# Performance work log

Measured on AMD Instinct MI355X. Metric: run time of the kernel, lower is better.

Reference implementation:

```python
import math
import jax, jax.numpy as jnp
import numpy as np

EPS = 1e-4
FMAX = 18  # max filtersize for scale clamped to 2.5: ceil(3*2^2.5+0.5)=18 -> kernel 37x37
KSZ = 2 * FMAX + 1


def _conv2d(x, w, b):
    # 3x3 conv, padding 1, NCHW / OIHW (cross-correlation, matches torch)
    y = jax.lax.conv_general_dilated(x, w, (1, 1), [(1, 1), (1, 1)],
                                     dimension_numbers=('NCHW', 'OIHW', 'NCHW'))
    return y + b[None, :, None, None]


def _basis_filters(scale):
    # scale: [B] -> [B,3,K,K] (g, dgdx, dgdy), masked to the per-sample support
    std = 2.0 ** scale                              # [B]
    fs = jnp.ceil(3.0 * std + 0.5)                  # per-sample filtersize
    x = jnp.arange(-FMAX, FMAX + 1, dtype=jnp.float32)          # [K]
    m = (jnp.abs(x)[None, :] <= fs[:, None]).astype(jnp.float32)  # [B,K] support mask
    e = jnp.exp(-0.5 * (x[None, :] / std[:, None]) ** 2) * m      # masked 1D gaussian [B,K]
    g = e[:, :, None] * e[:, None, :]                              # [B,K,K]
    g = g / jnp.sum(g, axis=(1, 2), keepdims=True)
    c = (-x[None, :] / (std[:, None] ** 3 * 2.0 * math.pi)) * e    # [B,K]
    dgdx = c[:, :, None] * e[:, None, :]   # varies along first spatial dim (x[0])
    dgdx = dgdx / jnp.sum(jnp.abs(dgdx), axis=(1, 2), keepdims=True)
    dgdy = e[:, :, None] * c[:, None, :]   # varies along second spatial dim (x[1])
    dgdy = dgdy / jnp.sum(jnp.abs(dgdy), axis=(1, 2), keepdims=True)
    return jnp.stack([g, dgdx, dgdy], axis=1)  # [B,3,K,K]


def setup_inputs() -> dict:
    key = jax.random.key(0)
    ks = jax.random.split(key, 7)
    B, H, W = 8, 512, 512
    batch = jax.random.uniform(ks[0], (B, 3, H, W), dtype=jnp.float32)
    gcm = jnp.array([[0.06, 0.63, 0.27], [0.3, 0.04, -0.35], [0.34, -0.6, 0.17]],
                    dtype=jnp.float32)
    w1 = jax.random.normal(ks[1], (16, 3, 3, 3), dtype=jnp.float32) * 0.1
    b1 = jax.random.normal(ks[2], (16,), dtype=jnp.float32) * 0.01
    w2 = jax.random.normal(ks[3], (16, 16, 3, 3), dtype=jnp.float32) * 0.1
    b2 = jax.random.normal(ks[4], (16,), dtype=jnp.float32) * 0.01
    w3 = jax.random.normal(ks[5], (1, 16, 3, 3), dtype=jnp.float32) * 0.1
    b3 = jax.random.normal(ks[6], (1,), dtype=jnp.float32) * 0.01
    return {"batch": batch, "gcm": gcm, "w1": w1, "b1": b1,
            "w2": w2, "b2": b2, "w3": w3, "b3": b3}


def reference(batch, gcm, w1, b1, w2, b2, w3, b3):
    B, _, H, W = batch.shape
    # ---- RGB order prior (non-differentiable, no_grad in torch) ----
    oh = lambda i: jax.nn.one_hot(i, 3, axis=1, dtype=batch.dtype)
    mx = jnp.argmax(batch, axis=1)                 # first max
    mn = jnp.argmin(batch, axis=1)
    bf = batch[:, ::-1]
    mx2 = 2 - jnp.argmax(bf, axis=1)               # last max
    mn2 = 2 - jnp.argmin(bf, axis=1)
    RGB_order = jax.lax.stop_gradient(
        0.5 * (oh(mx) + oh(mx2)) - 0.5 * (oh(mn) + oh(mn2)))  # [B,3,H,W]

    # ---- per-sample adaptive scale from small CNN ----
    h = jax.nn.silu(_conv2d(batch, w1, b1))
    h = jax.nn.silu(_conv2d(h, w2, b2))
    s = _conv2d(h, w3, b3)
    scale = jnp.clip(jnp.mean(s, axis=(1, 2, 3)), -2.5, 2.5)   # [B]

    # ---- Gaussian color model ----
    xg = jnp.einsum('ij,bjhw->bihw', gcm, batch)  # [B,3,H,W] -> (E, El, Ell)

    # ---- per-sample Gaussian basis convolution, batched via grouped conv ----
    basis = _basis_filters(scale)                                  # [B,3,K,K]
    xin = xg.reshape(1, B * 3, H, W)
    wk = jnp.broadcast_to(basis[:, None], (B, 3, 3, KSZ, KSZ)).reshape(B * 9, 1, KSZ, KSZ)
    out = jax.lax.conv_general_dilated(xin, wk, (1, 1), [(FMAX, FMAX), (FMAX, FMAX)],
                                       feature_group_count=B * 3,
                                       dimension_numbers=('NCHW', 'OIHW', 'NCHW'))
    out = out.reshape(B, 3, 3, H, W)   # [B, chan(E/El/Ell), filt(g/dx/dy), H, W]
    E = out[:, 0, 0:1]
    Ex = out[:, 0, 1:2]
    Ey = out[:, 0, 2:3]
    El = out[:, 1, 0:1]
    Ell = out[:, 2, 0:1]

    Hf = jnp.arctan(El / (Ell + EPS))
    S = jnp.log((El ** 2 + Ell ** 2) / (E ** 2 + EPS) + EPS)
    Ww = jnp.arctan((Ex / (E + EPS)) ** 2 + (Ey / (E + EPS)) ** 2)
    return jnp.concatenate([Hf, S, RGB_order, Ww], axis=1)  # [B,6,H,W]
```

## Files before the change

### kernel.cpp

```cpp
#include <hip/hip_runtime.h>
#include <hip/hip_bf16.h>

constexpr int BN = 8, HH = 512, WW = 512;
constexpr int PIX = HH * WW;
constexpr float EPSF = 1e-4f;

__device__ __forceinline__ float b2f(__hip_bfloat16 x) { return __bfloat162float(x); }
__device__ __forceinline__ __hip_bfloat16 f2b(float x) { return __float2bfloat16(x); }
__device__ __forceinline__ unsigned short bfbits(float x) {
    union { __hip_bfloat16 b; unsigned short u; } cv; cv.b = f2b(x); return cv.u;
}
__device__ __forceinline__ float ubf(unsigned short u) {
    union { unsigned int i; float f; } c; c.i = ((unsigned int)u) << 16; return c.f;
}
__device__ __forceinline__ unsigned int cvtpk(float lo, float hi) {
    unsigned int r;
    asm("v_cvt_pk_bf16_f32 %0, %1, %2" : "=v"(r) : "v"(lo), "v"(hi));
    return r;
}
__device__ __forceinline__ float silu(float a) {
    return a * __builtin_amdgcn_rcpf(1.f + __expf(-a));
}

typedef __attribute__((ext_vector_type(8))) short bf16x8;
typedef __attribute__((ext_vector_type(4))) float f32x4;

#define MF(acc, A, B) (acc) = __builtin_amdgcn_mfma_f32_16x16x32_bf16((A), (B), (acc), 0, 0, 0)

__device__ __forceinline__ bf16x8 ldb(const unsigned short* s, int off16) {
    const uint2* p = (const uint2*)(s + off16);
    uint2 a = p[0], c = p[1];
    union { uint4 u; bf16x8 v; } cv;
    cv.u = make_uint4(a.x, a.y, c.x, c.y);
    return cv.v;
}

constexpr int OFF_TOT = 0;
constexpr int OFF_ROW0 = 128;
constexpr int OFF_ROW1 = 256;
constexpr int OFF_COL0 = 384;
constexpr int OFF_COL1 = 512;
constexpr int OFF_COR = 640;
constexpr int OFF_W1R = 1280;
constexpr int OFF_WR  = 2048;
constexpr int OFF_AFR = 8192;
constexpr int OFF_PART = 32768;
constexpr size_t OFF_TP0 = 393216;
constexpr size_t SZ_TPH = (size_t)BN * PIX * 2;
constexpr size_t SZ_TPF = (size_t)BN * PIX * 4;
constexpr size_t OFF_TP1 = OFF_TP0 + SZ_TPH;
constexpr size_t OFF_TP2 = OFF_TP1 + SZ_TPF;
constexpr size_t OFF_TP3 = OFF_TP2 + SZ_TPF;
constexpr size_t WS_NEEDED = OFF_TP3 + SZ_TPH;

__global__ void prep_kernel(const float* __restrict__ w1, const float* __restrict__ w2,
                            float* __restrict__ wsf) {
    int t = threadIdx.x;
    for (int i = t; i < 640; i += 256) wsf[i] = 0.f;
    unsigned short* ab = (unsigned short*)(wsf + OFF_WR);
    for (int idx = t; idx < 5120; idx += 256) {
        int part = idx / 2560;
        int id = idx - part * 2560;
        int ks = id >> 9, rem = id & 511, lane = rem >> 3, j = id & 7;
        int oc = lane & 15, q = lane >> 4;
        int k = q * 8 + j;
        int tap = 2 * ks + (k >> 4), ic = k & 15;
        float val = (tap <= 8) ? w2[oc * 144 + ic * 9 + tap] : 0.f;
        float hv = b2f(f2b(val));
        ab[idx] = (part == 0) ? bfbits(val) : bfbits(val - hv);
    }
    unsigned short* a1 = (unsigned short*)(wsf + OFF_W1R);
    for (int idx = t; idx < 1024; idx += 256) {
        int part = idx >> 9;
        int id = idx & 511;
        int lane = id >> 3, j = id & 7;
        int oc = lane & 15, q = lane >> 4;
        int k = q * 8 + j;
        float val = (k < 27) ? w1[oc * 27 + k] : 0.f;
        float hv = b2f(f2b(val));
        a1[idx] = (part == 0) ? bfbits(val) : bfbits(val - hv);
    }
}

__global__ __launch_bounds__(256) void conv12_kernel(const float* __restrict__ batch,
                                                     const unsigned short* __restrict__ w1buf,
                                                     const float* __restrict__ b1,
                                                     const unsigned short* __restrict__ abuf,
                                                     const float* __restrict__ b2v,
                                                     float* __restrict__ wsf,
                                                     float* __restrict__ out) {
    __shared__ unsigned short stb[3][12][68];
    __shared__ uint4 h1s[10 * 66 * 2];
    __shared__ float part[4][16];

    int tx = threadIdx.x;
    int lane = tx & 63, wave = tx >> 6;
    int n = lane & 15, q = lane >> 4;
    int w0 = blockIdx.x * 64, h0 = blockIdx.y * 8, b = blockIdx.z;

    union { uint4 u; bf16x8 v; } cv;
    const float* pb = batch + (size_t)(b * 3) * PIX;

    unsigned int* stw = (unsigned int*)&stb[0][0][0];
    for (int i = tx; i < 1224; i += 256) {
        int ch = i / 408, rem = i - ch * 408;
        int r = rem / 34, c2 = rem - r * 34;
        int gh = h0 - 2 + r, gw = w0 - 2 + 2 * c2;
        const float* p = pb + (size_t)ch * PIX + (size_t)gh * WW;
        bool rok = (gh >= 0) && (gh < HH);
        float v0 = (rok && gw >= 0 && gw < WW) ? p[gw] : 0.f;
        float v1 = (rok && gw + 1 >= 0 && gw + 1 < WW) ? p[gw + 1] : 0.f;
        stw[i] = cvtpk(v0, v1);
    }

    bf16x8 w1h, w1l;
    const uint4* w14 = (const uint4*)w1buf;
    cv.u = w14[lane];      w1h = cv.v;
    cv.u = w14[64 + lane]; w1l = cv.v;
    int koff[8];
#pragma unroll
    for (int j = 0; j < 8; j++) {
        int k = q * 8 + j;
        int kk = (k < 27) ? k : 0;
        int ic = kk / 9, rem = kk - ic * 9, kh = rem / 3, kw = rem - kh * 3;
        koff[j] = ic * 816 + kh * 68 + kw;
    }
    float b1q[4];
#pragma unroll
    for (int r = 0; r < 4; r++) b1q[r] = b1[q * 4 + r];
    bool hiq = (q == 3);
    __syncthreads();

    const unsigned short* sptr = &stb[0][0][0];
    unsigned int* hw = (unsigned int*)h1s;
    union U8 { unsigned short h[8]; unsigned int w[4]; bf16x8 v; };
    int i_c = wave * 16 + n;
    int r_c = (unsigned)i_c / 66u; int c_c = i_c - r_c * 66;
    int base_c = r_c * 68 + c_c;
    U8 curv;
#pragma unroll
    for (int j = 0; j < 8; j++) curv.h[j] = sptr[base_c + koff[j]];
    for (int gi = 0; gi < 11; gi++) {
        U8 nxtv;
        int i_n = 0, r_n = 0, c_n = 0, base_n = 0;
        if (gi < 10) {
            i_n = i_c + 64;
            int wrap = (c_c >= 2);
            c_n = wrap ? (c_c - 2) : (c_c + 64);
            r_n = r_c + wrap;
            base_n = base_c + (wrap ? 66 : 64);
            if (i_n > 659) { i_n = 659; r_n = 9; c_n = 65; base_n = 677; }
#pragma unroll
            for (int j = 0; j < 8; j++) nxtv.h[j] = sptr[base_n + koff[j]];
        } else {
#pragma unroll
            for (int j = 0; j < 4; j++) nxtv.w[j] = 0u;
        }
        if (hiq) {
            curv.w[1] &= 0xFFFFu; curv.w[2] = 0u; curv.w[3] = 0u;
        }
        f32x4 a = {0, 0, 0, 0};
        MF(a, w1h, curv.v);
        MF(a, w1l, curv.v);
        int gh = h0 - 1 + r_c, gw = w0 - 1 + c_c;
        bool ok = ((unsigned)gh < (unsigned)HH) && ((unsigned)gw < (unsigned)WW);
        unsigned int p0 = cvtpk(silu(a[0] + b1q[0]), silu(a[1] + b1q[1]));
        unsigned int p1 = cvtpk(silu(a[2] + b1q[2]), silu(a[3] + b1q[3]));
        p0 = ok ? p0 : 0u;
        p1 = ok ? p1 : 0u;
        int swz = (c_c >> 2) & 1;
        int slot = i_c * 2 + ((q >= 2) ? (swz ^ 1) : swz);
        *(uint2*)&hw[slot * 4 + (q & 1) * 2] = make_uint2(p0, p1);
        curv = nxtv;
        i_c = i_n; r_c = r_n; c_c = c_n; base_c = base_n;
    }

    for (int j = tx; j < 512; j += 256) {
        int rr = j >> 6, ccx = j & 63;
        size_t p = (size_t)(h0 + rr) * WW + (w0 + ccx);
        float v0 = pb[p], v1 = pb[(size_t)PIX + p], v2 = pb[2 * (size_t)PIX + p];
        int mx  = (v0 >= v1 && v0 >= v2) ? 0 : ((v1 >= v2) ? 1 : 2);
        int mx2 = (v2 >= v1 && v2 >= v0) ? 2 : ((v1 >= v0) ? 1 : 0);
        int mn  = (v0 <= v1 && v0 <= v2) ? 0 : ((v1 <= v2) ? 1 : 2);
        int mn2 = (v2 <= v1 && v2 <= v0) ? 2 : ((v1 <= v0) ? 1 : 0);
#pragma unroll
        for (int c = 0; c < 3; c++) {
            float r = 0.5f * ((float)(c == mx) + (float)(c == mx2))
                    - 0.5f * ((float)(c == mn) + (float)(c == mn2));
            out[(size_t)(b * 6 + 2 + c) * PIX + p] = r;
        }
    }
    __syncthreads();

    bf16x8 ah[5], al[5];
    const uint4* ab4 = (const uint4*)abuf;
#pragma unroll
    for (int ks = 0; ks < 5; ks++) {
        cv.u = ab4[ks * 64 + lane];       ah[ks] = cv.v;
        cv.u = ab4[320 + ks * 64 + lane]; al[ks] = cv.v;
    }
    float b2q[4];
#pragma unroll
    for (int r = 0; r < 4; r++) b2q[r] = b2v[q * 4 + r];
    int halfb = q & 1;

    float tt[4] = {0, 0, 0, 0};
    float cs0[4] = {0, 0, 0, 0};
    float cs1[4] = {0, 0, 0, 0};
    for (int rloc = 0; rloc < 2; rloc++) {
        int row = wave * 2 + rloc;
        int grow = h0 + row;
        f32x4 acc[4] = {{0,0,0,0},{0,0,0,0},{0,0,0,0},{0,0,0,0}};
#pragma unroll
        for (int ks = 0; ks < 5; ks++) {
            int tap = 2 * ks + (q >> 1); if (tap > 8) tap = 8;
            int dh = tap / 3 - 1, dw = tap % 3 - 1;
            int lr = row + 1 + dh;
            int c0 = 1 + dw + n;
            const uint4* pp = &h1s[(lr * 66 + c0) * 2 + (halfb ^ ((c0 >> 2) & 1))];
            bf16x8 B[4];
#pragma unroll
            for (int t = 0; t < 4; t++) { cv.u = pp[t * 32]; B[t] = cv.v; }
#pragma unroll
            for (int t = 0; t < 4; t++) { MF(acc[t], ah[ks], B[t]); MF(acc[t], al[ks], B[t]); }
        }
        float sv[4][4];
#pragma unroll
        for (int t = 0; t < 4; t++)
#pragma unroll
            for (int r = 0; r < 4; r++)
                sv[t][r] = silu(acc[t][r] + b2q[r]);
#pragma unroll
        for (int r = 0; r < 4; r++) tt[r] += sv[0][r] + sv[1][r] + sv[2][r] + sv[3][r];
        if (grow == 0 || grow == HH - 1) {
            int off = (grow == 0) ? OFF_ROW0 : OFF_ROW1;
#pragma unroll
            for (int r = 0; r < 4; r++) {
                float x = sv[0][r] + sv[1][r] + sv[2][r] + sv[3][r];
#pragma unroll
                for (int d = 1; d < 16; d <<= 1) x += __shfl_xor(x, d, 64);
                if (n == 0) atomicAdd(&wsf[off + b * 16 + q * 4 + r], x);
            }
        }
        if (blockIdx.x == 0 && n == 0)
#pragma unroll
            for (int r = 0; r < 4; r++) cs0[r] += sv[0][r];
        if (blockIdx.x == 7 && n == 15)
#pragma unroll
            for (int r = 0; r < 4; r++) cs1[r] += sv[3][r];
        if ((grow == 0 || grow == HH - 1)) {
            int hi = (grow == 0) ? 0 : 1;
            if (blockIdx.x == 0 && n == 0)
#pragma unroll
                for (int r = 0; r < 4; r++)
                    wsf[OFF_COR + ((b * 2 + hi) * 2 + 0) * 16 + q * 4 + r] = sv[0][r];
            if (blockIdx.x == 7 && n == 15)
#pragma unroll
                for (int r = 0; r < 4; r++)
                    wsf[OFF_COR + ((b * 2 + hi) * 2 + 1) * 16 + q * 4 + r] = sv[3][r];
        }
    }
    if (blockIdx.x == 0 && n == 0)
#pragma unroll
        for (int r = 0; r < 4; r++) atomicAdd(&wsf[OFF_COL0 + b * 16 + q * 4 + r], cs0[r]);
    if (blockIdx.x == 7 && n == 15)
#pragma unroll
        for (int r = 0; r < 4; r++) atomicAdd(&wsf[OFF_COL1 + b * 16 + q * 4 + r], cs1[r]);
#pragma unroll
    for (int r = 0; r < 4; r++) {
        float x = tt[r];
#pragma unroll
        for (int d = 1; d < 16; d <<= 1) x += __shfl_xor(x, d, 64);
        tt[r] = x;
    }
    if (n == 0)
#pragma unroll
        for (int r = 0; r < 4; r++) part[wave][q * 4 + r] = tt[r];
    __syncthreads();
    if (tx < 16) {
        int blk = blockIdx.y * 8 + blockIdx.x;
        wsf[OFF_PART + ((size_t)b * 512 + blk) * 16 + tx] =
            part[0][tx] + part[1][tx] + part[2][tx] + part[3][tx];
    }
}

__global__ void filter_kernel(const float* __restrict__ w3, const float* __restrict__ b3,
                              float* __restrict__ wsf) {
    int b = blockIdx.x, t = threadIdx.x;
    __shared__ float spart[128];
    __shared__ float stot[16];
    if (t < 128) {
        int ic = t & 15, ch = t >> 4;
        const float* pp = wsf + OFF_PART + ((size_t)b * 512 + ch * 64) * 16 + ic;
        float s = 0.f;
        for (int k = 0; k < 64; k++) s += pp[k * 16];
        spart[t] = s;
    }
    __syncthreads();
    if (t < 16) {
        float a = 0.f;
        for (int c2 = 0; c2 < 8; c2++) a += spart[c2 * 16 + t];
        stot[t] = a;
    }
    __syncthreads();
    __shared__ float red[160];
    float val = 0.f;
    if (t < 144) {
        int ic = t / 9, tap = t % 9, kh = tap / 3, kw = tap % 3;
        float T = stot[ic];
        int hi = -1, wi = -1;
        if (kh == 0) { T -= wsf[OFF_ROW1 + b * 16 + ic]; hi = 1; }
        else if (kh == 2) { T -= wsf[OFF_ROW0 + b * 16 + ic]; hi = 0; }
        if (kw == 0) { T -= wsf[OFF_COL1 + b * 16 + ic]; wi = 1; }
        else if (kw == 2) { T -= wsf[OFF_COL0 + b * 16 + ic]; wi = 0; }
        if (hi >= 0 && wi >= 0) T += wsf[OFF_COR + ((b * 2 + hi) * 2 + wi) * 16 + ic];
        val = w3[t] * T;
    }
    red[t] = val;
    __syncthreads();
    __shared__ float sh_mean;
    if (t == 0) {
        float S = 0.f;
        for (int i = 0; i < 144; i++) S += red[i];
        sh_mean = b3[0] + S * (1.f / (float)PIX);
    }
    __syncthreads();
    float scale = fminf(2.5f, fmaxf(-2.5f, sh_mean));
    float sd = exp2f(scale);
    float fs = ceilf(3.f * sd + 0.5f);
    float e = 0.f, c = 0.f;
    if (t < 37) {
        float x = (float)(t - 18);
        if (fabsf(x) <= fs) {
            float qq = x / sd;
            e = __expf(-0.5f * qq * qq);
            c = -x / (sd * sd * sd * 6.28318530717958647692f) * e;
        }
    }
    __shared__ float sa[40], sb2[40];
    if (t < 37) { sa[t] = e; sb2[t] = fabsf(c); }
    __syncthreads();
    __shared__ float Se, Sc;
    if (t == 0) {
        float a = 0.f, d = 0.f;
        for (int i = 0; i < 37; i++) { a += sa[i]; d += sb2[i]; }
        Se = a; Sc = d;
    }
    __syncthreads();
    __shared__ float sEn[37], sCn[37];
    if (t < 37) { sEn[t] = e / Se; sCn[t] = c / Sc; }
    __syncthreads();
    if (t < 64) {
        int r = t & 15, q = t >> 4;
        uint4* afr = (uint4*)(wsf + OFF_AFR) + (size_t)b * 640 + t;
#pragma unroll
        for (int ks = 0; ks < 2; ks++) {
            unsigned short eh[8], em[8], el[8], chp[8], cmp[8];
#pragma unroll
            for (int j2 = 0; j2 < 8; j2++) {
                int d = ks * 32 + q * 8 + j2 - r;
                bool ok = (d >= 0) && (d <= 36);
                float ve = ok ? sEn[ok ? d : 0] : 0.f;
                float vc = ok ? sCn[ok ? d : 0] : 0.f;
                eh[j2] = bfbits(ve);
                float r1 = ve - ubf(eh[j2]);
                em[j2] = bfbits(r1);
                el[j2] = bfbits(r1 - ubf(em[j2]));
                chp[j2] = bfbits(vc);
                cmp[j2] = bfbits(vc - ubf(chp[j2]));
            }
#define PK2(a0, a1) ((unsigned)(a0) | ((unsigned)(a1) << 16))
            afr[(ks * 3 + 0) * 64] = make_uint4(PK2(eh[0], eh[1]), PK2(eh[2], eh[3]), PK2(eh[4], eh[5]), PK2(eh[6], eh[7]));
            afr[(ks * 3 + 1) * 64] = make_uint4(PK2(em[0], em[1]), PK2(em[2], em[3]), PK2(em[4], em[5]), PK2(em[6], em[7]));
            afr[(ks * 3 + 2) * 64] = make_uint4(PK2(el[0], el[1]), PK2(el[2], el[3]), PK2(el[4], el[5]), PK2(el[6], el[7]));
            afr[(6 + ks * 2 + 0) * 64] = make_uint4(PK2(chp[0], chp[1]), PK2(chp[2], chp[3]), PK2(chp[4], chp[5]), PK2(chp[6], chp[7]));
            afr[(6 + ks * 2 + 1) * 64] = make_uint4(PK2(cmp[0], cmp[1]), PK2(cmp[2], cmp[3]), PK2(cmp[4], cmp[5]), PK2(cmp[6], cmp[7]));
#undef PK2
        }
    }
}

__global__ __launch_bounds__(256) void horiz_kernel(const float* __restrict__ batch,
                                                    const float* __restrict__ gcm,
                                                    const float* __restrict__ wsf,
                                                    unsigned short* __restrict__ tp0,
                                                    float* __restrict__ tp1,
                                                    float* __restrict__ tp2,
                                                    unsigned short* __restrict__ tp3) {
    __shared__ unsigned short sx[7 * 32 * 84];
    int tx = threadIdx.x;
    int lane = tx & 63, wave = tx >> 6;
    int n = lane & 15, q = lane >> 4;
    int j0 = blockIdx.x * 32, h0 = blockIdx.y * 32, b = blockIdx.z;
    const float* pb = batch + (size_t)(b * 3) * PIX;
    float g0 = gcm[0], g1 = gcm[1], g2 = gcm[2];
    float g3 = gcm[3], g4 = gcm[4], g5 = gcm[5];
    float g6 = gcm[6], g7 = gcm[7], g8 = gcm[8];
    for (int it = 0; it < 3; it++) {
        int qi = tx + it * 256;
        if (qi < 640) {
            int hh = qi / 20, qc = qi - hh * 20;
            int sc0 = qc * 4;
            int gc0 = j0 - 18 + sc0;
            const float* prow = pb + (size_t)(h0 + hh) * WW;
            float v0[4], v1[4], v2[4];
            if (gc0 >= 0 && gc0 + 3 < WW) {
                float2 a0 = *(const float2*)(prow + gc0);
                float2 a1 = *(const float2*)(prow + gc0 + 2);
                float2 b0 = *(const float2*)(prow + PIX + gc0);
                float2 b1 = *(const float2*)(prow + PIX + gc0 + 2);
                float2 c0 = *(const float2*)(prow + 2 * (size_t)PIX + gc0);
                float2 c1 = *(const float2*)(prow + 2 * (size_t)PIX + gc0 + 2);
                v0[0] = a0.x; v0[1] = a0.y; v0[2] = a1.x; v0[3] = a1.y;
                v1[0] = b0.x; v1[1] = b0.y; v1[2] = b1.x; v1[3] = b1.y;
                v2[0] = c0.x; v2[1] = c0.y; v2[2] = c1.x; v2[3] = c1.y;
            } else {
#pragma unroll
                for (int e = 0; e < 4; e++) {
                    int gc = gc0 + e;
                    bool okc = (unsigned)gc < (unsigned)WW;
                    v0[e] = okc ? prow[gc] : 0.f;
                    v1[e] = okc ? prow[(size_t)PIX + gc] : 0.f;
                    v2[e] = okc ? prow[2 * (size_t)PIX + gc] : 0.f;
                }
            }
            unsigned short x0b[4], h1b[4], m1b[4], l1b[4], h2b[4], m2b[4], l2b[4];
#pragma unroll
            for (int e = 0; e < 4; e++) {
                float x0 = g0 * v0[e] + g1 * v1[e] + g2 * v2[e];
                float x1 = g3 * v0[e] + g4 * v1[e] + g5 * v2[e];
                float x2 = g6 * v0[e] + g7 * v1[e] + g8 * v2[e];
                x0b[e] = bfbits(x0);
                h1b[e] = bfbits(x1); float r1 = x1 - ubf(h1b[e]);
                m1b[e] = bfbits(r1); l1b[e] = bfbits(r1 - ubf(m1b[e]));
                h2b[e] = bfbits(x2); float r2 = x2 - ubf(h2b[e]);
                m2b[e] = bfbits(r2); l2b[e] = bfbits(r2 - ubf(m2b[e]));
            }
            int o = hh * 84 + sc0;
            *(ushort4*)&sx[o]            = make_ushort4(x0b[0], x0b[1], x0b[2], x0b[3]);
            *(ushort4*)&sx[2688 + o]     = make_ushort4(h1b[0], h1b[1], h1b[2], h1b[3]);
            *(ushort4*)&sx[2 * 2688 + o] = make_ushort4(m1b[0], m1b[1], m1b[2], m1b[3]);
            *(ushort4*)&sx[3 * 2688 + o] = make_ushort4(l1b[0], l1b[1], l1b[2], l1b[3]);
            *(ushort4*)&sx[4 * 2688 + o] = make_ushort4(h2b[0], h2b[1], h2b[2], h2b[3]);
            *(ushort4*)&sx[5 * 2688 + o] = make_ushort4(m2b[0], m2b[1], m2b[2], m2b[3]);
            *(ushort4*)&sx[6 * 2688 + o] = make_ushort4(l2b[0], l2b[1], l2b[2], l2b[3]);
        }
    }
    const uint4* afr = (const uint4*)(wsf + OFF_AFR) + (size_t)b * 640 + lane;
    union { uint4 u; bf16x8 v; } cv;
    bf16x8 Ae[2][3], Ac[2][2];
#pragma unroll
    for (int ks = 0; ks < 2; ks++) {
#pragma unroll
        for (int p = 0; p < 3; p++) { cv.u = afr[(ks * 3 + p) * 64]; Ae[ks][p] = cv.v; }
#pragma unroll
        for (int p = 0; p < 2; p++) { cv.u = afr[(6 + ks * 2 + p) * 64]; Ac[ks][p] = cv.v; }
    }
    __syncthreads();
    int jt = wave & 1, ht = wave >> 1;
    f32x4 a0 = {0,0,0,0}, a1 = {0,0,0,0}, a2 = {0,0,0,0}, a3 = {0,0,0,0};
    int rb = (ht * 16 + n) * 84 + jt * 16 + q * 8;
#pragma unroll
    for (int ks = 0; ks < 2; ks++) {
        int rk = rb + ks * 32;
        bf16x8 B0  = ldb(sx, rk);
        bf16x8 B1h = ldb(sx, 2688 + rk), B1m = ldb(sx, 2 * 2688 + rk), B1l = ldb(sx, 3 * 2688 + rk);
        bf16x8 B2h = ldb(sx, 4 * 2688 + rk), B2m = ldb(sx, 5 * 2688 + rk), B2l = ldb(sx, 6 * 2688 + rk);
        MF(a0, Ae[ks][0], B0); MF(a0, Ae[ks][1], B0);
        MF(a3, Ac[ks][0], B0); MF(a3, Ac[ks][1], B0);
        MF(a1, Ae[ks][0], B1h); MF(a1, Ae[ks][0], B1m); MF(a1, Ae[ks][1], B1h);
        MF(a1, Ae[ks][0], B1l); MF(a1, Ae[ks][2], B1h); MF(a1, Ae[ks][1], B1m);
        MF(a2, Ae[ks][0], B2h); MF(a2, Ae[ks][0], B2m); MF(a2, Ae[ks][1], B2h);
        MF(a2, Ae[ks][0], B2l); MF(a2, Ae[ks][2], B2h); MF(a2, Ae[ks][1], B2m);
    }
    int jo = j0 + jt * 16 + q * 4;
    int ho = h0 + ht * 16 + n;
#pragma unroll
    for (int r = 0; r < 4; r++) {
        size_t ix = ((size_t)b * 512 + (jo + r)) * 512 + ho;
        tp0[ix] = bfbits(a0[r]);
        tp1[ix] = a1[r];
        tp2[ix] = a2[r];
        tp3[ix] = bfbits(a3[r]);
    }
}

__global__ __launch_bounds__(256) void vert_kernel(const float* __restrict__ wsf,
                                                   const unsigned short* __restrict__ tp0,
                                                   const float* __restrict__ tp1,
                                                   const float* __restrict__ tp2,
                                                   const unsigned short* __restrict__ tp3,
                                                   float* __restrict__ out) {
    __shared__ unsigned short sb[8 * 32 * 84];
    int tx = threadIdx.x;
    int lane = tx & 63, wave = tx >> 6;
    int n = lane & 15, q = lane >> 4;
    int j0 = blockIdx.x * 32, r0 = blockIdx.y * 32, b = blockIdx.z;
    for (int it = 0; it < 3; it++) {
        int qi = tx + it * 256;
        if (qi < 640) {
            int jj = qi / 20, qc = qi - jj * 20;
            int sr0 = qc * 4;
            int gh0 = r0 - 18 + sr0;
            size_t ixb = ((size_t)b * 512 + (j0 + jj)) * 512;
            unsigned int t0a, t0b, t3a, t3b;
            float f1[4], f2[4];
            if (gh0 >= 0 && gh0 + 3 < HH) {
                size_t ix0 = ixb + gh0;
                t0a = *(const unsigned int*)&tp0[ix0];
                t0b = *(const unsigned int*)&tp0[ix0 + 2];
                t3a = *(const unsigned int*)&tp3[ix0];
                t3b = *(const unsigned int*)&tp3[ix0 + 2];
                float2 fa = *(const float2*)&tp1[ix0];
                float2 fb = *(const float2*)&tp1[ix0 + 2];
                float2 fc = *(const float2*)&tp2[ix0];
                float2 fd = *(const float2*)&tp2[ix0 + 2];
                f1[0] = fa.x; f1[1] = fa.y; f1[2] = fb.x; f1[3] = fb.y;
                f2[0] = fc.x; f2[1] = fc.y; f2[2] = fd.x; f2[3] = fd.y;
            } else {
                unsigned short u0[4] = {0, 0, 0, 0}, u3[4] = {0, 0, 0, 0};
#pragma unroll
                for (int e = 0; e < 4; e++) {
                    f1[e] = 0.f; f2[e] = 0.f;
                    int gh = gh0 + e;
                    if ((unsigned)gh < (unsigned)HH) {
                        size_t ix = ixb + gh;
                        u0[e] = tp0[ix]; f1[e] = tp1[ix]; f2[e] = tp2[ix]; u3[e] = tp3[ix];
                    }
                }
                t0a = (unsigned)u0[0] | ((unsigned)u0[1] << 16);
                t0b = (unsigned)u0[2] | ((unsigned)u0[3] << 16);
                t3a = (unsigned)u3[0] | ((unsigned)u3[1] << 16);
                t3b = (unsigned)u3[2] | ((unsigned)u3[3] << 16);
            }
            unsigned short h1b[4], m1b[4], l1b[4], h2b[4], m2b[4], l2b[4];
#pragma unroll
            for (int e = 0; e < 4; e++) {
                h1b[e] = bfbits(f1[e]); float r1 = f1[e] - ubf(h1b[e]);
                m1b[e] = bfbits(r1); l1b[e] = bfbits(r1 - ubf(m1b[e]));
                h2b[e] = bfbits(f2[e]); float r2 = f2[e] - ubf(h2b[e]);
                m2b[e] = bfbits(r2); l2b[e] = bfbits(r2 - ubf(m2b[e]));
            }
            int o = jj * 84 + sr0;
            *(uint2*)&sb[o] = make_uint2(t0a, t0b);
            *(ushort4*)&sb[2688 + o]     = make_ushort4(h1b[0], h1b[1], h1b[2], h1b[3]);
            *(ushort4*)&sb[2 * 2688 + o] = make_ushort4(m1b[0], m1b[1], m1b[2], m1b[3]);
            *(ushort4*)&sb[3 * 2688 + o] = make_ushort4(l1b[0], l1b[1], l1b[2], l1b[3]);
            *(ushort4*)&sb[4 * 2688 + o] = make_ushort4(h2b[0], h2b[1], h2b[2], h2b[3]);
            *(ushort4*)&sb[5 * 2688 + o] = make_ushort4(m2b[0], m2b[1], m2b[2], m2b[3]);
            *(ushort4*)&sb[6 * 2688 + o] = make_ushort4(l2b[0], l2b[1], l2b[2], l2b[3]);
            *(uint2*)&sb[7 * 2688 + o] = make_uint2(t3a, t3b);
        }
    }
    const uint4* afr = (const uint4*)(wsf + OFF_AFR) + (size_t)b * 640 + lane;
    union { uint4 u; bf16x8 v; } cv;
    bf16x8 Ae[2][3], Ac[2][2];
#pragma unroll
    for (int ks = 0; ks < 2; ks++) {
#pragma unroll
        for (int p = 0; p < 3; p++) { cv.u = afr[(ks * 3 + p) * 64]; Ae[ks][p] = cv.v; }
#pragma unroll
        for (int p = 0; p < 2; p++) { cv.u = afr[(6 + ks * 2 + p) * 64]; Ac[ks][p] = cv.v; }
    }
    __syncthreads();
    int ct = wave & 1, rt = wave >> 1;
    f32x4 aE = {0,0,0,0}, aX = {0,0,0,0}, aY = {0,0,0,0}, aL = {0,0,0,0}, aLL = {0,0,0,0};
    int rb = (ct * 16 + n) * 84 + rt * 16 + q * 8;
#pragma unroll
    for (int ks = 0; ks < 2; ks++) {
        int rk = rb + ks * 32;
        bf16x8 B0  = ldb(sb, rk);
        bf16x8 B1h = ldb(sb, 2688 + rk), B1m = ldb(sb, 2 * 2688 + rk), B1l = ldb(sb, 3 * 2688 + rk);
        bf16x8 B2h = ldb(sb, 4 * 2688 + rk), B2m = ldb(sb, 5 * 2688 + rk), B2l = ldb(sb, 6 * 2688 + rk);
        bf16x8 B3  = ldb(sb, 7 * 2688 + rk);
        MF(aE, Ae[ks][0], B0); MF(aE, Ae[ks][1], B0);
        MF(aX, Ac[ks][0], B0); MF(aX, Ac[ks][1], B0);
        MF(aY, Ae[ks][0], B3); MF(aY, Ae[ks][1], B3);
        MF(aL, Ae[ks][0], B1h); MF(aL, Ae[ks][0], B1m); MF(aL, Ae[ks][1], B1h);
        MF(aL, Ae[ks][0], B1l); MF(aL, Ae[ks][2], B1h); MF(aL, Ae[ks][1], B1m);
        MF(aLL, Ae[ks][0], B2h); MF(aLL, Ae[ks][0], B2m); MF(aLL, Ae[ks][1], B2h);
        MF(aLL, Ae[ks][0], B2l); MF(aLL, Ae[ks][2], B2h); MF(aLL, Ae[ks][1], B2m);
    }
    int ho = r0 + rt * 16 + q * 4;
    int jo = j0 + ct * 16 + n;
#pragma unroll
    for (int r = 0; r < 4; r++) {
        float E = aE[r], Ex = aX[r], Ey = aY[r], El = aL[r], Ell = aLL[r];
        float Hf = atanf(El / (Ell + EPSF));
        float S = logf((El * El + Ell * Ell) / (E * E + EPSF) + EPSF);
        float rx = Ex / (E + EPSF), ry = Ey / (E + EPSF);
        float Wv = atanf(rx * rx + ry * ry);
        size_t base = (size_t)(b * 6) * PIX + (size_t)(ho + r) * WW + jo;
        out[base] = Hf;
        out[base + PIX] = S;
        out[base + 5 * (size_t)PIX] = Wv;
    }
}

extern "C" void kernel_launch(void* const* d_in, const int* in_sizes, int n_in,
                              void* d_out, int out_size, void* d_ws, size_t ws_size,
                              hipStream_t stream) {
    const float* batch = (const float*)d_in[0];
    const float* gcm   = (const float*)d_in[1];
    const float* w1    = (const float*)d_in[2];
    const float* b1    = (const float*)d_in[3];
    const float* w2    = (const float*)d_in[4];
    const float* b2    = (const float*)d_in[5];
    const float* w3    = (const float*)d_in[6];
    const float* b3    = (const float*)d_in[7];
    float* out = (float*)d_out;

    if (ws_size < WS_NEEDED) return;

    float* wsf = (float*)d_ws;
    unsigned short* tp0 = (unsigned short*)((char*)d_ws + OFF_TP0);
    float* tp1 = (float*)((char*)d_ws + OFF_TP1);
    float* tp2 = (float*)((char*)d_ws + OFF_TP2);
    unsigned short* tp3 = (unsigned short*)((char*)d_ws + OFF_TP3);

    prep_kernel<<<dim3(1), dim3(256), 0, stream>>>(w1, w2, wsf);
    conv12_kernel<<<dim3(8, 64, 8), dim3(256), 0, stream>>>(
        batch, (const unsigned short*)(wsf + OFF_W1R), b1,
        (const unsigned short*)(wsf + OFF_WR), b2, wsf, out);
    filter_kernel<<<dim3(8), dim3(160), 0, stream>>>(w3, b3, wsf);
    horiz_kernel<<<dim3(16, 16, 8), dim3(256), 0, stream>>>(batch, gcm, wsf, tp0, tp1, tp2, tp3);
    vert_kernel<<<dim3(16, 16, 8), dim3(256), 0, stream>>>(wsf, tp0, tp1, tp2, tp3, out);
}
```

Measured before the change: 229.5 us.

## Drop prep kernel: pack weights in-kernel and replace boundary atomics with partials

Removes the single-block prep kernel, which zeroed the atomic accumulators and pre-packed the w1/w2 bf16 hi/lo fragments. Each conv12 block now builds those fragments itself from the fp32 weights. The row and column boundary sums are written as per-block partials instead of atomicAdds, which removes the need for zeroing, and filter_kernel reduces those partials. This saves one launch and the serialization it causes, at the cost of redundant weight conversion in every block and a longer reduction in filter_kernel. OFF_COR is still read in filter_kernel but is no longer zeroed by prep, so the corner terms may depend on whether conv12 writes them rather than accumulating into them.

```diff
diff --git a/kernel.cpp b/kernel.cpp
--- a/kernel.cpp
+++ b/kernel.cpp
@@ -35,17 +35,14 @@
     return cv.v;
 }
 
-constexpr int OFF_TOT = 0;
-constexpr int OFF_ROW0 = 128;
-constexpr int OFF_ROW1 = 256;
-constexpr int OFF_COL0 = 384;
-constexpr int OFF_COL1 = 512;
 constexpr int OFF_COR = 640;
-constexpr int OFF_W1R = 1280;
-constexpr int OFF_WR  = 2048;
-constexpr int OFF_AFR = 8192;
-constexpr int OFF_PART = 32768;
-constexpr size_t OFF_TP0 = 393216;
+constexpr int OFF_PR0 = 1280;
+constexpr int OFF_PR1 = 2304;
+constexpr int OFF_PC0 = 3328;
+constexpr int OFF_PC1 = 36096;
+constexpr int OFF_AFR = 69632;
+constexpr int OFF_PART = 90112;
+constexpr size_t OFF_TP0 = 655360;
 constexpr size_t SZ_TPH = (size_t)BN * PIX * 2;
 constexpr size_t SZ_TPF = (size_t)BN * PIX * 4;
 constexpr size_t OFF_TP1 = OFF_TP0 + SZ_TPH;
@@ -53,39 +50,10 @@
 constexpr size_t OFF_TP3 = OFF_TP2 + SZ_TPF;
 constexpr size_t WS_NEEDED = OFF_TP3 + SZ_TPH;
 
-__global__ void prep_kernel(const float* __restrict__ w1, const float* __restrict__ w2,
-                            float* __restrict__ wsf) {
-    int t = threadIdx.x;
-    for (int i = t; i < 640; i += 256) wsf[i] = 0.f;
-    unsigned short* ab = (unsigned short*)(wsf + OFF_WR);
-    for (int idx = t; idx < 5120; idx += 256) {
-        int part = idx / 2560;
-        int id = idx - part * 2560;
-        int ks = id >> 9, rem = id & 511, lane = rem >> 3, j = id & 7;
-        int oc = lane & 15, q = lane >> 4;
-        int k = q * 8 + j;
-        int tap = 2 * ks + (k >> 4), ic = k & 15;
-        float val = (tap <= 8) ? w2[oc * 144 + ic * 9 + tap] : 0.f;
-        float hv = b2f(f2b(val));
-        ab[idx] = (part == 0) ? bfbits(val) : bfbits(val - hv);
-    }
-    unsigned short* a1 = (unsigned short*)(wsf + OFF_W1R);
-    for (int idx = t; idx < 1024; idx += 256) {
-        int part = idx >> 9;
-        int id = idx & 511;
-        int lane = id >> 3, j = id & 7;
-        int oc = lane & 15, q = lane >> 4;
-        int k = q * 8 + j;
-        float val = (k < 27) ? w1[oc * 27 + k] : 0.f;
-        float hv = b2f(f2b(val));
-        a1[idx] = (part == 0) ? bfbits(val) : bfbits(val - hv);
-    }
-}
-
 __global__ __launch_bounds__(256) void conv12_kernel(const float* __restrict__ batch,
-                                                     const unsigned short* __restrict__ w1buf,
+                                                     const float* __restrict__ w1,
                                                      const float* __restrict__ b1,
-                                                     const unsigned short* __restrict__ abuf,
+                                                     const float* __restrict__ w2,
                                                      const float* __restrict__ b2v,
                                                      float* __restrict__ wsf,
                                                      float* __restrict__ out) {
@@ -114,9 +82,22 @@
     }
 
     bf16x8 w1h, w1l;
-    const uint4* w14 = (const uint4*)w1buf;
-    cv.u = w14[lane];      w1h = cv.v;
-    cv.u = w14[64 + lane]; w1l = cv.v;
+    {
+        int oc = lane & 15;
+        union { unsigned int w[4]; bf16x8 v; } fh, fl;
+#pragma unroll
+        for (int jp = 0; jp < 4; jp++) {
+            int k0 = q * 8 + 2 * jp, k1 = k0 + 1;
+            float v0 = (k0 < 27) ? w1[oc * 27 + k0] : 0.f;
+            float v1 = (k1 < 27) ? w1[oc * 27 + k1] : 0.f;
+            unsigned int hi = cvtpk(v0, v1);
+            float h0f = ubf((unsigned short)(hi & 0xFFFFu));
+            float h1f = ubf((unsigned short)(hi >> 16));
+            fh.w[jp] = hi;
+            fl.w[jp] = cvtpk(v0 - h0f, v1 - h1f);
+        }
+        w1h = fh.v; w1l = fl.v;
+    }
     int koff[8];
 #pragma unroll
     for (int j = 0; j < 8; j++) {
@@ -193,11 +174,26 @@
     __syncthreads();
 
     bf16x8 ah[5], al[5];
-    const uint4* ab4 = (const uint4*)abuf;
-#pragma unroll
-    for (int ks = 0; ks < 5; ks++) {
-        cv.u = ab4[ks * 64 + lane];       ah[ks] = cv.v;
-        cv.u = ab4[320 + ks * 64 + lane]; al[ks] = cv.v;
+    {
+        int oc = lane & 15;
+#pragma unroll
+        for (int ks = 0; ks < 5; ks++) {
+            union { unsigned int w[4]; bf16x8 v; } fh, fl;
+#pragma unroll
+            for (int jp = 0; jp < 4; jp++) {
+                int k0 = q * 8 + 2 * jp, k1 = k0 + 1;
+                int tap0 = 2 * ks + (k0 >> 4), ic0 = k0 & 15;
+                int tap1 = 2 * ks + (k1 >> 4), ic1 = k1 & 15;
+                float v0 = (tap0 <= 8) ? w2[oc * 144 + ic0 * 9 + tap0] : 0.f;
+                float v1 = (tap1 <= 8) ? w2[oc * 144 + ic1 * 9 + tap1] : 0.f;
+                unsigned int hi = cvtpk(v0, v1);
+                float h0f = ubf((unsigned short)(hi & 0xFFFFu));
+                float h1f = ubf((unsigned short)(hi >> 16));
+                fh.w[jp] = hi;
+                fl.w[jp] = cvtpk(v0 - h0f, v1 - h1f);
+            }
+            ah[ks] = fh.v; al[ks] = fl.v;
+        }
     }
     float b2q[4];
 #pragma unroll
@@ -233,13 +229,13 @@
 #pragma unroll
         for (int r = 0; r < 4; r++) tt[r] += sv[0][r] + sv[1][r] + sv[2][r] + sv[3][r];
         if (grow == 0 || grow == HH - 1) {
-            int off = (grow == 0) ? OFF_ROW0 : OFF_ROW1;
+            int off = (grow == 0) ? OFF_PR0 : OFF_PR1;
 #pragma unroll
             for (int r = 0; r < 4; r++) {
                 float x = sv[0][r] + sv[1][r] + sv[2][r] + sv[3][r];
 #pragma unroll
                 for (int d = 1; d < 16; d <<= 1) x += __shfl_xor(x, d, 64);
-                if (n == 0) atomicAdd(&wsf[off + b * 16 + q * 4 + r], x);
+                if (n == 0) wsf[off + (b * 8 + (int)blockIdx.x) * 16 + q * 4 + r] = x;
             }
         }
         if (blockIdx.x == 0 && n == 0)
@@ -262,10 +258,12 @@
     }
     if (blockIdx.x == 0 && n == 0)
 #pragma unroll
-        for (int r = 0; r < 4; r++) atomicAdd(&wsf[OFF_COL0 + b * 16 + q * 4 + r], cs0[r]);
+        for (int r = 0; r < 4; r++)
+            wsf[OFF_PC0 + (((size_t)b * 64 + blockIdx.y) * 4 + wave) * 16 + q * 4 + r] = cs0[r];
     if (blockIdx.x == 7 && n == 15)
 #pragma unroll
-        for (int r = 0; r < 4; r++) atomicAdd(&wsf[OFF_COL1 + b * 16 + q * 4 + r], cs1[r]);
+        for (int r = 0; r < 4; r++)
+            wsf[OFF_PC1 + (((size_t)b * 64 + blockIdx.y) * 4 + wave) * 16 + q * 4 + r] = cs1[r];
 #pragma unroll
     for (int r = 0; r < 4; r++) {
         float x = tt[r];
@@ -288,7 +286,7 @@
                               float* __restrict__ wsf) {
     int b = blockIdx.x, t = threadIdx.x;
     __shared__ float spart[128];
-    __shared__ float stot[16];
+    __shared__ float stot[16], sr0[16], sr1[16], sc0v[16], sc1v[16];
     if (t < 128) {
         int ic = t & 15, ch = t >> 4;
         const float* pp = wsf + OFF_PART + ((size_t)b * 512 + ch * 64) * 16 + ic;
@@ -302,6 +300,44 @@
         for (int c2 = 0; c2 < 8; c2++) a += spart[c2 * 16 + t];
         stot[t] = a;
     }
+    if (t >= 16 && t < 32) {
+        int ic = t - 16; float s = 0.f;
+        for (int i = 0; i < 8; i++) s += wsf[OFF_PR0 + (b * 8 + i) * 16 + ic];
+        sr0[ic] = s;
+    }
+    if (t >= 32 && t < 48) {
+        int ic = t - 32; float s = 0.f;
+        for (int i = 0; i < 8; i++) s += wsf[OFF_PR1 + (b * 8 + i) * 16 + ic];
+        sr1[ic] = s;
+    }
+    __syncthreads();
+    if (t < 128) {
+        int ic = t & 15, ch = t >> 4;
+        const float* pp = wsf + OFF_PC0 + ((size_t)b * 256 + ch * 32) * 16 + ic;
+        float s = 0.f;
+        for (int k = 0; k < 32; k++) s += pp[k * 16];
+        spart[t] = s;
+    }
+    __syncthreads();
+    if (t < 16) {
+        float a = 0.f;
+        for (int c2 = 0; c2 < 8; c2++) a += spart[c2 * 16 + t];
+        sc0v[t] = a;
+    }
+    __syncthreads();
+    if (t < 128) {
+        int ic = t & 15, ch = t >> 4;
+        const float* pp = wsf + OFF_PC1 + ((size_t)b * 256 + ch * 32) * 16 + ic;
+        float s = 0.f;
+        for (int k = 0; k < 32; k++) s += pp[k * 16];
+        spart[t] = s;
+    }
+    __syncthreads();
+    if (t < 16) {
+        float a = 0.f;
+        for (int c2 = 0; c2 < 8; c2++) a += spart[c2 * 16 + t];
+        sc1v[t] = a;
+    }
     __syncthreads();
     __shared__ float red[160];
     float val = 0.f;
@@ -309,10 +345,10 @@
         int ic = t / 9, tap = t % 9, kh = tap / 3, kw = tap % 3;
         float T = stot[ic];
         int hi = -1, wi = -1;
-        if (kh == 0) { T -= wsf[OFF_ROW1 + b * 16 + ic]; hi = 1; }
-        else if (kh == 2) { T -= wsf[OFF_ROW0 + b * 16 + ic]; hi = 0; }
-        if (kw == 0) { T -= wsf[OFF_COL1 + b * 16 + ic]; wi = 1; }
-        else if (kw == 2) { T -= wsf[OFF_COL0 + b * 16 + ic]; wi = 0; }
+        if (kh == 0) { T -= sr1[ic]; hi = 1; }
+        else if (kh == 2) { T -= sr0[ic]; hi = 0; }
+        if (kw == 0) { T -= sc1v[ic]; wi = 1; }
+        else if (kw == 2) { T -= sc0v[ic]; wi = 0; }
         if (hi >= 0 && wi >= 0) T += wsf[OFF_COR + ((b * 2 + hi) * 2 + wi) * 16 + ic];
         val = w3[t] * T;
     }
@@ -618,10 +654,8 @@
     float* tp2 = (float*)((char*)d_ws + OFF_TP2);
     unsigned short* tp3 = (unsigned short*)((char*)d_ws + OFF_TP3);
 
-    prep_kernel<<<dim3(1), dim3(256), 0, stream>>>(w1, w2, wsf);
     conv12_kernel<<<dim3(8, 64, 8), dim3(256), 0, stream>>>(
-        batch, (const unsigned short*)(wsf + OFF_W1R), b1,
-        (const unsigned short*)(wsf + OFF_WR), b2, wsf, out);
+        batch, w1, b1, w2, b2, wsf, out);
     filter_kernel<<<dim3(8), dim3(160), 0, stream>>>(w3, b3, wsf);
     horiz_kernel<<<dim3(16, 16, 8), dim3(256), 0, stream>>>(batch, gcm, wsf, tp0, tp1, tp2, tp3);
     vert_kernel<<<dim3(16, 16, 8), dim3(256), 0, stream>>>(wsf, tp0, tp1, tp2, tp3, out);
```

Measured after the change: 230.8 us. About the same (+0.6%).
